# Kernel tuning notes

Hardware: AMD Instinct MI355X
Metric: run time of the kernel (lower is better)

Reference implementation:

```python
import jax, jax.numpy as jnp
import numpy as np

HEADS = 8  # init kwarg
EPS = 1e-5  # torch LayerNorm default


def layer_norm(x, g, b):
    m = jnp.mean(x, axis=-1, keepdims=True)
    v = jnp.mean((x - m) ** 2, axis=-1, keepdims=True)
    return (x - m) * jax.lax.rsqrt(v + EPS) * g + b


def setup_inputs() -> dict:
    key = jax.random.key(0)
    B, N, H, DS = 16, 1024, 256, 3
    ks = jax.random.split(key, 12)
    s = 0.02
    return {
        "x_source": jax.random.normal(ks[0], (B, N, H), jnp.float32),
        "p_source": jax.random.normal(ks[1], (B, N, DS), jnp.float32),
        "x_out": jax.random.normal(ks[2], (B, N, H), jnp.float32),
        "p_out": jax.random.normal(ks[3], (B, N, DS), jnp.float32),
        # LayerNorm params (norm_conv_source / norm_conv_out)
        "g_s": jnp.ones((H,), jnp.float32),
        "b_s": jnp.zeros((H,), jnp.float32),
        "g_o": jnp.ones((H,), jnp.float32),
        "b_o": jnp.zeros((H,), jnp.float32),
        # CovariantAttention params: QKV act on the [.., 2H] concat
        "Wq": jax.random.normal(ks[4], (2 * H, H), jnp.float32) * s,
        "Wk": jax.random.normal(ks[5], (2 * H, H), jnp.float32) * s,
        "Wv": jax.random.normal(ks[6], (2 * H, H), jnp.float32) * s,
        "Wo": jax.random.normal(ks[7], (H, H), jnp.float32) * s,
        # position head (update_p=True, d_space=3)
        "Wp": jax.random.normal(ks[8], (H, DS), jnp.float32) * s,
    }


def reference(x_source, p_source, x_out, p_out, g_s, b_s, g_o, b_o, Wq, Wk, Wv, Wo, Wp):
    B, N, H = x_out.shape
    dh = H // HEADS
    # dual LayerNorm + concat
    xs = layer_norm(x_source, g_s, b_s)
    xo = layer_norm(x_out, g_o, b_o)
    f = jnp.concatenate([xs, xo], axis=-1)  # [B, N, 2H]
    # covariant cross-attention (reconstructed CovariantAttention)
    q = (f @ Wq).reshape(B, N, HEADS, dh)
    k = (f @ Wk).reshape(B, N, HEADS, dh)
    v = (f @ Wv).reshape(B, N, HEADS, dh)
    scores = jnp.einsum("bqhd,bkhd->bhqk", q, k) / jnp.sqrt(jnp.asarray(dh, f.dtype))
    alpha = jax.nn.softmax(scores, axis=-1)  # [B, heads, N, N]
    msg = jnp.einsum("bhqk,bkhd->bqhd", alpha, v).reshape(B, N, H)
    m_x_out = msg @ Wo
    # residual feature update + position head (update_p=True)
    x_out_new = x_out + m_x_out
    p_out_new = m_x_out @ Wp
    return (x_out_new, p_out_new)
```

## Files before the change

kernel.cpp:

```cpp
#include <hip/hip_runtime.h>
#include <hip/hip_bf16.h>

#define B_ 16
#define N_ 1024
#define H_ 256
#define HEADS_ 8
#define DH_ 32
#define BN_ (B_*N_)
#define F_ (2*H_)
#define QKV_ 768

typedef __attribute__((ext_vector_type(8))) __bf16 bf16x8;
typedef __attribute__((ext_vector_type(4))) float floatx4;

#define QSC 0.25506910542339896f

#if __has_builtin(__builtin_amdgcn_exp2f)
#define EXP2(x) __builtin_amdgcn_exp2f(x)
#else
#define EXP2(x) exp2f(x)
#endif

__device__ __forceinline__ unsigned short f2bf(float f) {
    union { float f; unsigned int u; } c; c.f = f;
    unsigned int u = c.u;
    return (unsigned short)((u + 0x7fffu + ((u >> 16) & 1u)) >> 16);
}
__device__ __forceinline__ float bf2f(unsigned short s) {
    union { unsigned int u; float f; } c; c.u = ((unsigned int)s) << 16;
    return c.f;
}
__device__ __forceinline__ unsigned int fbits(float f) {
    union { float f; unsigned int u; } c; c.f = f; return c.u;
}
__device__ __forceinline__ unsigned int pk2(float lo, float hi) {
    return __builtin_amdgcn_perm(fbits(hi) + 0x8000u, fbits(lo) + 0x8000u, 0x07060302u);
}

__device__ __forceinline__ void async16(const void* g, void* l) {
    __builtin_amdgcn_global_load_lds(
        (const __attribute__((address_space(1))) unsigned int*)g,
        (__attribute__((address_space(3))) unsigned int*)l,
        16, 0, 0);
}

__global__ __launch_bounds__(256) void prep(
        const float* __restrict__ xs_g, const float* __restrict__ xo_g,
        const float* __restrict__ gs, const float* __restrict__ bs,
        const float* __restrict__ go, const float* __restrict__ bo,
        const float* __restrict__ Wq, const float* __restrict__ Wk,
        const float* __restrict__ Wv, const float* __restrict__ Wo,
        const float* __restrict__ Wp,
        unsigned short* __restrict__ f,
        unsigned short* __restrict__ WcT, unsigned short* __restrict__ WoT,
        float* __restrict__ WoP) {
    if (blockIdx.x < 4096) {
        int t = threadIdx.x & 63;
        int row = blockIdx.x * 4 + (threadIdx.x >> 6);
        const float4 vs = ((const float4*)(xs_g + (size_t)row * H_))[t];
        const float4 vo = ((const float4*)(xo_g + (size_t)row * H_))[t];
        float s1 = vs.x + vs.y + vs.z + vs.w;
        float s2 = vs.x*vs.x + vs.y*vs.y + vs.z*vs.z + vs.w*vs.w;
        float o1 = vo.x + vo.y + vo.z + vo.w;
        float o2 = vo.x*vo.x + vo.y*vo.y + vo.z*vo.z + vo.w*vo.w;
        #pragma unroll
        for (int m = 1; m < 64; m <<= 1) {
            s1 += __shfl_xor(s1, m); s2 += __shfl_xor(s2, m);
            o1 += __shfl_xor(o1, m); o2 += __shfl_xor(o2, m);
        }
        const float inv = 1.0f / 256.0f;
        float ms = s1 * inv, vvs = s2 * inv - ms * ms;
        float mo = o1 * inv, vvo = o2 * inv - mo * mo;
        float rs = rsqrtf(vvs + 1e-5f);
        float ro = rsqrtf(vvo + 1e-5f);
        float4 g4s = ((const float4*)gs)[t];
        float4 b4s = ((const float4*)bs)[t];
        float4 g4o = ((const float4*)go)[t];
        float4 b4o = ((const float4*)bo)[t];
        ushort4 os, oo;
        os.x = f2bf((vs.x - ms) * rs * g4s.x + b4s.x);
        os.y = f2bf((vs.y - ms) * rs * g4s.y + b4s.y);
        os.z = f2bf((vs.z - ms) * rs * g4s.z + b4s.z);
        os.w = f2bf((vs.w - ms) * rs * g4s.w + b4s.w);
        oo.x = f2bf((vo.x - mo) * ro * g4o.x + b4o.x);
        oo.y = f2bf((vo.y - mo) * ro * g4o.y + b4o.y);
        oo.z = f2bf((vo.z - mo) * ro * g4o.z + b4o.z);
        oo.w = f2bf((vo.w - mo) * ro * g4o.w + b4o.w);
        *(ushort4*)(f + (size_t)row * F_ + 4 * t) = os;
        *(ushort4*)(f + (size_t)row * F_ + H_ + 4 * t) = oo;
    } else {
        int i = (blockIdx.x - 4096) * 256 + threadIdx.x;
        const int total1 = QKV_ * F_;
        if (i < total1) {
            int n = i / F_, k = i % F_;
            float w;
            if (n < 256)      w = Wq[(size_t)k * H_ + n];
            else if (n < 512) w = Wk[(size_t)k * H_ + (n - 256)];
            else              w = Wv[(size_t)k * H_ + (n - 512)];
            WcT[i] = f2bf(w);
        }
        const int total2 = H_ * H_;
        if (i < total2) {
            int n = i / H_, k = i % H_;
            WoT[i] = f2bf(Wo[(size_t)k * H_ + n]);
        }
        if (i < H_ * 3) {
            int c = i / 3, j = i % 3;
            float s = 0.f;
            for (int n = 0; n < H_; ++n) s += Wo[(size_t)c * H_ + n] * Wp[n * 3 + j];
            WoP[i] = s;
        }
    }
}

__global__ __launch_bounds__(256) void qkv_gemm(
        const unsigned short* __restrict__ f,
        const unsigned short* __restrict__ WcT,
        unsigned short* __restrict__ qb,
        unsigned short* __restrict__ kb,
        unsigned short* __restrict__ vT) {
    __shared__ __align__(16) unsigned short As[128 * 32];
    __shared__ __align__(16) unsigned short Bs[128 * 32];
    int t = threadIdx.x;
    int w = t >> 6, lane = t & 63;
    int r = lane & 15, qd = lane >> 4;
    int wm = (w >> 1) * 64, wn = (w & 1) * 64;
    int m0 = blockIdx.y * 128, n0 = blockIdx.x * 128;
    int lrow = lane >> 2, lcol = (lane & 3) * 8;
    floatx4 acc[4][4] = {};
    const unsigned short* gA = f   + (size_t)(m0 + w * 32 + lrow) * F_ + lcol;
    const unsigned short* gB = WcT + (size_t)(n0 + w * 32 + lrow) * F_ + lcol;
    unsigned short* lA = As + (w * 32) * 32;
    unsigned short* lB = Bs + (w * 32) * 32;
    for (int k0 = 0; k0 < F_; k0 += 32) {
        async16(gA + k0,            lA);
        async16(gA + k0 + 16 * F_,  lA + 16 * 32);
        async16(gB + k0,            lB);
        async16(gB + k0 + 16 * F_,  lB + 16 * 32);
        __syncthreads();
        bf16x8 aF[4], bF[4];
        #pragma unroll
        for (int mt = 0; mt < 4; ++mt)
            aF[mt] = *(const bf16x8*)(As + (wm + mt * 16 + r) * 32 + qd * 8);
        #pragma unroll
        for (int nt = 0; nt < 4; ++nt)
            bF[nt] = *(const bf16x8*)(Bs + (wn + nt * 16 + r) * 32 + qd * 8);
        #pragma unroll
        for (int mt = 0; mt < 4; ++mt)
            #pragma unroll
            for (int nt = 0; nt < 4; ++nt)
                acc[mt][nt] = __builtin_amdgcn_mfma_f32_16x16x32_bf16(aF[mt], bF[nt], acc[mt][nt], 0, 0, 0);
        __syncthreads();
    }
    #pragma unroll
    for (int nt = 0; nt < 4; ++nt) {
        int cg = n0 + wn + nt * 16 + r;
        int sec = cg >> 8;
        int hh = (cg >> 5) & 7;
        int d = cg & 31;
        #pragma unroll
        for (int mt = 0; mt < 4; ++mt) {
            int tok = m0 + wm + mt * 16 + qd * 4;
            int b = tok >> 10, tl = tok & 1023;
            size_t hb = (size_t)b * 8 + hh;
            if (sec == 0) {
                unsigned short* p = qb + (hb * 1024 + tl) * 32 + d;
                #pragma unroll
                for (int i = 0; i < 4; ++i) p[i * 32] = f2bf(acc[mt][nt][i] * QSC);
            } else if (sec == 1) {
                unsigned short* p = kb + (hb * 1024 + tl) * 32 + d;
                #pragma unroll
                for (int i = 0; i < 4; ++i) p[i * 32] = f2bf(acc[mt][nt][i]);
            } else {
                ushort4 v4;
                v4.x = f2bf(acc[mt][nt][0]); v4.y = f2bf(acc[mt][nt][1]);
                v4.z = f2bf(acc[mt][nt][2]); v4.w = f2bf(acc[mt][nt][3]);
                *(ushort4*)(vT + (hb * 32 + d) * 1024 + tl) = v4;
            }
        }
    }
}

__global__ __launch_bounds__(256) void attn(
        const unsigned short* __restrict__ qb,
        const unsigned short* __restrict__ kb,
        const unsigned short* __restrict__ vT,
        unsigned short* __restrict__ msg) {
    __shared__ float ob[4][32][66];
    __shared__ float lb[4][64];
    int blk = blockIdx.x;
    int qt = blk & 15;
    int h  = (blk >> 4) & 7;
    int b  = blk >> 7;
    int t = threadIdx.x;
    int w = t >> 6, lane = t & 63;
    int r = lane & 15, qd = lane >> 4;
    int q0 = qt * 64;
    size_t hb = (size_t)b * 8 + h;
    const unsigned short* qs = qb + hb * (1024 * 32);
    const unsigned short* ks = kb + hb * (1024 * 32);
    const unsigned short* vs = vT + hb * (32 * 1024);
    bf16x8 qf[4];
    #pragma unroll
    for (int i = 0; i < 4; ++i)
        qf[i] = *(const bf16x8*)(qs + (size_t)(q0 + i * 16 + r) * 32 + qd * 8);
    union { unsigned int u[4]; bf16x8 v; } onesu;
    onesu.u[0] = onesu.u[1] = onesu.u[2] = onesu.u[3] = 0x3F803F80u;
    const bf16x8 onesv = onesu.v;
    floatx4 o0[4] = {}, o1[4] = {}, ol[4] = {};
    int srcA = ((qd & 1) * 2) * 16 + r;
    int srcB = srcA + 16;
    bool hiq = qd >= 2;
    int kb0 = w * 256;
    for (int kc = 0; kc < 256; kc += 32) {
        int kk = kb0 + kc;
        bf16x8 kf0 = *(const bf16x8*)(ks + (size_t)(kk + r) * 32 + qd * 8);
        bf16x8 kf1 = *(const bf16x8*)(ks + (size_t)(kk + 16 + r) * 32 + qd * 8);
        bf16x8 vf0 = *(const bf16x8*)(vs + (size_t)r * 1024 + kk + qd * 8);
        bf16x8 vf1 = *(const bf16x8*)(vs + (size_t)(16 + r) * 1024 + kk + qd * 8);
        #pragma unroll
        for (int i = 0; i < 4; ++i) {
            floatx4 z = {0.f,0.f,0.f,0.f};
            floatx4 s0 = __builtin_amdgcn_mfma_f32_16x16x32_bf16(kf0, qf[i], z, 0, 0, 0);
            floatx4 s1 = __builtin_amdgcn_mfma_f32_16x16x32_bf16(kf1, qf[i], z, 0, 0, 0);
            float e0[4], e1[4];
            #pragma unroll
            for (int j = 0; j < 4; ++j) {
                e0[j] = EXP2(s0[j]);
                e1[j] = EXP2(s1[j]);
            }
            unsigned int t00 = pk2(e0[0], e0[1]), t01 = pk2(e0[2], e0[3]);
            unsigned int t10 = pk2(e1[0], e1[1]), t11 = pk2(e1[2], e1[3]);
            unsigned int a0 = __shfl((int)t00, srcA), a1 = __shfl((int)t01, srcA);
            unsigned int b0 = __shfl((int)t00, srcB), b1 = __shfl((int)t01, srcB);
            unsigned int c0 = __shfl((int)t10, srcA), c1 = __shfl((int)t11, srcA);
            unsigned int d0 = __shfl((int)t10, srcB), d1 = __shfl((int)t11, srcB);
            union { unsigned int u[4]; bf16x8 v; } pf;
            pf.u[0] = hiq ? c0 : a0;
            pf.u[1] = hiq ? c1 : a1;
            pf.u[2] = hiq ? d0 : b0;
            pf.u[3] = hiq ? d1 : b1;
            o0[i] = __builtin_amdgcn_mfma_f32_16x16x32_bf16(vf0, pf.v, o0[i], 0, 0, 0);
            o1[i] = __builtin_amdgcn_mfma_f32_16x16x32_bf16(vf1, pf.v, o1[i], 0, 0, 0);
            ol[i] = __builtin_amdgcn_mfma_f32_16x16x32_bf16(onesv, pf.v, ol[i], 0, 0, 0);
        }
    }
    #pragma unroll
    for (int i = 0; i < 4; ++i) {
        #pragma unroll
        for (int j = 0; j < 4; ++j) {
            ob[w][qd * 4 + j][i * 16 + r]      = o0[i][j];
            ob[w][16 + qd * 4 + j][i * 16 + r] = o1[i][j];
        }
        if (qd == 0) lb[w][i * 16 + r] = ol[i][0];
    }
    __syncthreads();
    {
        int q2 = t >> 2, dg = t & 3;
        float acc8[8] = {0.f,0.f,0.f,0.f,0.f,0.f,0.f,0.f};
        float L = 0.f;
        #pragma unroll
        for (int ww = 0; ww < 4; ++ww) {
            L += lb[ww][q2];
            #pragma unroll
            for (int j = 0; j < 8; ++j)
                acc8[j] += ob[ww][dg * 8 + j][q2];
        }
        float rinv = 1.0f / L;
        uint4 pkd;
        pkd.x = pk2(acc8[0] * rinv, acc8[1] * rinv);
        pkd.y = pk2(acc8[2] * rinv, acc8[3] * rinv);
        pkd.z = pk2(acc8[4] * rinv, acc8[5] * rinv);
        pkd.w = pk2(acc8[6] * rinv, acc8[7] * rinv);
        *(uint4*)(msg + ((size_t)(b * N_ + q0 + q2)) * H_ + h * DH_ + dg * 8) = pkd;
    }
}

__global__ __launch_bounds__(256) void out_gemm(
        const unsigned short* __restrict__ msg,
        const unsigned short* __restrict__ WoT,
        const float* __restrict__ x_out,
        float* __restrict__ outx) {
    __shared__ __align__(16) unsigned short As[64 * 32];
    __shared__ __align__(16) unsigned short Bs[64 * 32];
    int t = threadIdx.x;
    int w = t >> 6, lane = t & 63;
    int r = lane & 15, qd = lane >> 4;
    int wm = (w >> 1) * 32, wn = (w & 1) * 32;
    int m0 = blockIdx.y * 64, n0 = blockIdx.x * 64;
    int lrow = lane >> 2, lcol = (lane & 3) * 8;
    floatx4 acc[2][2] = {};
    const unsigned short* gA = msg + (size_t)(m0 + w * 16 + lrow) * H_ + lcol;
    const unsigned short* gB = WoT + (size_t)(n0 + w * 16 + lrow) * H_ + lcol;
    unsigned short* lA = As + (w * 16) * 32;
    unsigned short* lB = Bs + (w * 16) * 32;
    for (int k0 = 0; k0 < H_; k0 += 32) {
        async16(gA + k0, lA);
        async16(gB + k0, lB);
        __syncthreads();
        bf16x8 aF[2], bF[2];
        #pragma unroll
        for (int mt = 0; mt < 2; ++mt)
            aF[mt] = *(const bf16x8*)(As + (wm + mt * 16 + r) * 32 + qd * 8);
        #pragma unroll
        for (int nt = 0; nt < 2; ++nt)
            bF[nt] = *(const bf16x8*)(Bs + (wn + nt * 16 + r) * 32 + qd * 8);
        #pragma unroll
        for (int mt = 0; mt < 2; ++mt)
            #pragma unroll
            for (int nt = 0; nt < 2; ++nt)
                acc[mt][nt] = __builtin_amdgcn_mfma_f32_16x16x32_bf16(aF[mt], bF[nt], acc[mt][nt], 0, 0, 0);
        __syncthreads();
    }
    #pragma unroll
    for (int nt = 0; nt < 2; ++nt) {
        int cg = n0 + wn + nt * 16 + r;
        #pragma unroll
        for (int mt = 0; mt < 2; ++mt) {
            int tok = m0 + wm + mt * 16 + qd * 4;
            #pragma unroll
            for (int i = 0; i < 4; ++i) {
                size_t idx = (size_t)(tok + i) * H_ + cg;
                outx[idx] = x_out[idx] + acc[mt][nt][i];
            }
        }
    }
}

__global__ __launch_bounds__(64) void p_kernel(
        const unsigned short* __restrict__ msg, const float* __restrict__ WoP,
        float* __restrict__ outp) {
    int row = blockIdx.x;
    int t = threadIdx.x;
    float a0 = 0.f, a1 = 0.f, a2 = 0.f;
    #pragma unroll
    for (int i = 0; i < 4; ++i) {
        int c = t + 64 * i;
        float v = bf2f(msg[(size_t)row * H_ + c]);
        a0 += v * WoP[c * 3 + 0];
        a1 += v * WoP[c * 3 + 1];
        a2 += v * WoP[c * 3 + 2];
    }
    #pragma unroll
    for (int m = 1; m < 64; m <<= 1) {
        a0 += __shfl_xor(a0, m); a1 += __shfl_xor(a1, m); a2 += __shfl_xor(a2, m);
    }
    if (t == 0) {
        outp[(size_t)row * 3 + 0] = a0;
        outp[(size_t)row * 3 + 1] = a1;
        outp[(size_t)row * 3 + 2] = a2;
    }
}

extern "C" void kernel_launch(void* const* d_in, const int* in_sizes, int n_in,
                              void* d_out, int out_size, void* d_ws, size_t ws_size,
                              hipStream_t stream) {
    const float* x_source = (const float*)d_in[0];
    const float* x_out = (const float*)d_in[2];
    const float* g_s = (const float*)d_in[4];
    const float* b_s = (const float*)d_in[5];
    const float* g_o = (const float*)d_in[6];
    const float* b_o = (const float*)d_in[7];
    const float* Wq = (const float*)d_in[8];
    const float* Wk = (const float*)d_in[9];
    const float* Wv = (const float*)d_in[10];
    const float* Wo = (const float*)d_in[11];
    const float* Wp = (const float*)d_in[12];

    float* outx = (float*)d_out;
    float* outp = outx + (size_t)BN_ * H_;

    char* ws = (char*)d_ws;
    unsigned short* f_buf = (unsigned short*)(ws);
    unsigned short* WcT   = (unsigned short*)(ws + 16777216);
    unsigned short* WoT   = (unsigned short*)(ws + 17563648);
    float*          WoP   = (float*)         (ws + 17694720);
    unsigned short* qb    = (unsigned short*)(ws + 17697792);
    unsigned short* kb    = (unsigned short*)(ws + 26086400);
    unsigned short* vT    = (unsigned short*)(ws + 34475008);
    unsigned short* msg   = (unsigned short*)(ws + 42863616);

    prep<<<4096 + 1536, 256, 0, stream>>>(x_source, x_out, g_s, b_s, g_o, b_o,
                                          Wq, Wk, Wv, Wo, Wp, f_buf, WcT, WoT, WoP);
    {
        dim3 g(QKV_ / 128, BN_ / 128);
        qkv_gemm<<<g, 256, 0, stream>>>(f_buf, WcT, qb, kb, vT);
    }
    attn<<<B_ * HEADS_ * (N_ / 64), 256, 0, stream>>>(qb, kb, vT, msg);
    {
        dim3 g(H_ / 64, BN_ / 64);
        out_gemm<<<g, 256, 0, stream>>>(msg, WoT, x_out, outx);
    }
    p_kernel<<<BN_, 64, 0, stream>>>(msg, WoP, outp);
}
```

Measured before the change: 199.0 us.

## Fuse position head into output GEMM via MFMA and use hardware bf16 pack

Removes the separate p_kernel launch by computing the position projection inside out_gemm. Column-0 blocks issue extra MFMAs against a zero-padded bf16 copy of Wo·Wp, which costs a little extra work in those blocks and lowers the precision of the folded weights to bf16. The attention inner loop also switches its exp-result packing to the hardware cvt_pk_bf16_f32 instruction when available. That drops the manual rounding add, so the fallback path now truncates instead of rounding.

```diff
diff --git a/kernel.cpp b/kernel.cpp
--- a/kernel.cpp
+++ b/kernel.cpp
@@ -35,6 +35,16 @@
 }
 __device__ __forceinline__ unsigned int pk2(float lo, float hi) {
     return __builtin_amdgcn_perm(fbits(hi) + 0x8000u, fbits(lo) + 0x8000u, 0x07060302u);
+}
+__device__ __forceinline__ unsigned int pkp(float lo, float hi) {
+#if __has_builtin(__builtin_amdgcn_cvt_pk_bf16_f32)
+    typedef __attribute__((ext_vector_type(2))) __bf16 bf2;
+    union { bf2 v; unsigned int u; } c;
+    c.v = __builtin_amdgcn_cvt_pk_bf16_f32(lo, hi);
+    return c.u;
+#else
+    return __builtin_amdgcn_perm(fbits(hi), fbits(lo), 0x07060302u);
+#endif
 }
 
 __device__ __forceinline__ void async16(const void* g, void* l) {
@@ -53,7 +63,7 @@
         const float* __restrict__ Wp,
         unsigned short* __restrict__ f,
         unsigned short* __restrict__ WcT, unsigned short* __restrict__ WoT,
-        float* __restrict__ WoP) {
+        unsigned short* __restrict__ WpT) {
     if (blockIdx.x < 4096) {
         int t = threadIdx.x & 63;
         int row = blockIdx.x * 4 + (threadIdx.x >> 6);
@@ -104,11 +114,15 @@
             int n = i / H_, k = i % H_;
             WoT[i] = f2bf(Wo[(size_t)k * H_ + n]);
         }
-        if (i < H_ * 3) {
-            int c = i / 3, j = i % 3;
-            float s = 0.f;
-            for (int n = 0; n < H_; ++n) s += Wo[(size_t)c * H_ + n] * Wp[n * 3 + j];
-            WoP[i] = s;
+        if (i < 16 * H_) {
+            int n = i >> 8, k = i & 255;
+            if (n < 3) {
+                float s = 0.f;
+                for (int m = 0; m < H_; ++m) s += Wo[(size_t)k * H_ + m] * Wp[m * 3 + n];
+                WpT[i] = f2bf(s);
+            } else {
+                WpT[i] = 0;
+            }
         }
     }
 }
@@ -229,8 +243,8 @@
                 e0[j] = EXP2(s0[j]);
                 e1[j] = EXP2(s1[j]);
             }
-            unsigned int t00 = pk2(e0[0], e0[1]), t01 = pk2(e0[2], e0[3]);
-            unsigned int t10 = pk2(e1[0], e1[1]), t11 = pk2(e1[2], e1[3]);
+            unsigned int t00 = pkp(e0[0], e0[1]), t01 = pkp(e0[2], e0[3]);
+            unsigned int t10 = pkp(e1[0], e1[1]), t11 = pkp(e1[2], e1[3]);
             unsigned int a0 = __shfl((int)t00, srcA), a1 = __shfl((int)t01, srcA);
             unsigned int b0 = __shfl((int)t00, srcB), b1 = __shfl((int)t01, srcB);
             unsigned int c0 = __shfl((int)t10, srcA), c1 = __shfl((int)t11, srcA);
@@ -279,8 +293,9 @@
 __global__ __launch_bounds__(256) void out_gemm(
         const unsigned short* __restrict__ msg,
         const unsigned short* __restrict__ WoT,
+        const unsigned short* __restrict__ WpT,
         const float* __restrict__ x_out,
-        float* __restrict__ outx) {
+        float* __restrict__ outx, float* __restrict__ outp) {
     __shared__ __align__(16) unsigned short As[64 * 32];
     __shared__ __align__(16) unsigned short Bs[64 * 32];
     int t = threadIdx.x;
@@ -289,7 +304,9 @@
     int wm = (w >> 1) * 32, wn = (w & 1) * 32;
     int m0 = blockIdx.y * 64, n0 = blockIdx.x * 64;
     int lrow = lane >> 2, lcol = (lane & 3) * 8;
+    bool do_p = (blockIdx.x == 0) && ((w & 1) == 0);
     floatx4 acc[2][2] = {};
+    floatx4 accp[2] = {};
     const unsigned short* gA = msg + (size_t)(m0 + w * 16 + lrow) * H_ + lcol;
     const unsigned short* gB = WoT + (size_t)(n0 + w * 16 + lrow) * H_ + lcol;
     unsigned short* lA = As + (w * 16) * 32;
@@ -310,6 +327,12 @@
             #pragma unroll
             for (int nt = 0; nt < 2; ++nt)
                 acc[mt][nt] = __builtin_amdgcn_mfma_f32_16x16x32_bf16(aF[mt], bF[nt], acc[mt][nt], 0, 0, 0);
+        if (do_p) {
+            bf16x8 bP = *(const bf16x8*)(WpT + (size_t)r * H_ + k0 + qd * 8);
+            #pragma unroll
+            for (int mt = 0; mt < 2; ++mt)
+                accp[mt] = __builtin_amdgcn_mfma_f32_16x16x32_bf16(aF[mt], bP, accp[mt], 0, 0, 0);
+        }
         __syncthreads();
     }
     #pragma unroll
@@ -325,30 +348,14 @@
             }
         }
     }
-}
-
-__global__ __launch_bounds__(64) void p_kernel(
-        const unsigned short* __restrict__ msg, const float* __restrict__ WoP,
-        float* __restrict__ outp) {
-    int row = blockIdx.x;
-    int t = threadIdx.x;
-    float a0 = 0.f, a1 = 0.f, a2 = 0.f;
-    #pragma unroll
-    for (int i = 0; i < 4; ++i) {
-        int c = t + 64 * i;
-        float v = bf2f(msg[(size_t)row * H_ + c]);
-        a0 += v * WoP[c * 3 + 0];
-        a1 += v * WoP[c * 3 + 1];
-        a2 += v * WoP[c * 3 + 2];
-    }
-    #pragma unroll
-    for (int m = 1; m < 64; m <<= 1) {
-        a0 += __shfl_xor(a0, m); a1 += __shfl_xor(a1, m); a2 += __shfl_xor(a2, m);
-    }
-    if (t == 0) {
-        outp[(size_t)row * 3 + 0] = a0;
-        outp[(size_t)row * 3 + 1] = a1;
-        outp[(size_t)row * 3 + 2] = a2;
+    if (do_p && r < 3) {
+        #pragma unroll
+        for (int mt = 0; mt < 2; ++mt) {
+            int tok = m0 + wm + mt * 16 + qd * 4;
+            #pragma unroll
+            for (int i = 0; i < 4; ++i)
+                outp[(size_t)(tok + i) * 3 + r] = accp[mt][i];
+        }
     }
 }
 
@@ -374,14 +381,14 @@
     unsigned short* f_buf = (unsigned short*)(ws);
     unsigned short* WcT   = (unsigned short*)(ws + 16777216);
     unsigned short* WoT   = (unsigned short*)(ws + 17563648);
-    float*          WoP   = (float*)         (ws + 17694720);
-    unsigned short* qb    = (unsigned short*)(ws + 17697792);
-    unsigned short* kb    = (unsigned short*)(ws + 26086400);
-    unsigned short* vT    = (unsigned short*)(ws + 34475008);
-    unsigned short* msg   = (unsigned short*)(ws + 42863616);
+    unsigned short* WpT   = (unsigned short*)(ws + 17694720);
+    unsigned short* qb    = (unsigned short*)(ws + 17702912);
+    unsigned short* kb    = (unsigned short*)(ws + 26091520);
+    unsigned short* vT    = (unsigned short*)(ws + 34480128);
+    unsigned short* msg   = (unsigned short*)(ws + 42868736);
 
     prep<<<4096 + 1536, 256, 0, stream>>>(x_source, x_out, g_s, b_s, g_o, b_o,
-                                          Wq, Wk, Wv, Wo, Wp, f_buf, WcT, WoT, WoP);
+                                          Wq, Wk, Wv, Wo, Wp, f_buf, WcT, WoT, WpT);
     {
         dim3 g(QKV_ / 128, BN_ / 128);
         qkv_gemm<<<g, 256, 0, stream>>>(f_buf, WcT, qb, kb, vT);
@@ -389,7 +396,6 @@
     attn<<<B_ * HEADS_ * (N_ / 64), 256, 0, stream>>>(qb, kb, vT, msg);
     {
         dim3 g(H_ / 64, BN_ / 64);
-        out_gemm<<<g, 256, 0, stream>>>(msg, WoT, x_out, outx);
-    }
-    p_kernel<<<BN_, 64, 0, stream>>>(msg, WoP, outp);
-}
+        out_gemm<<<g, 256, 0, stream>>>(msg, WoT, WpT, x_out, outx, outp);
+    }
+}
```

Result: faster. 194.7 us (-2.1%).
